# Kernel optimization log

Measured on AMD Instinct MI355X. Metric: run time of the kernel, lower is better.

The kernel has to match this reference:

```python
import jax, jax.numpy as jnp
import numpy as np

TEMP_LP = 0.05  # args.temp_lp_loss


def setup_inputs() -> dict:
    key = jax.random.key(0)
    k1, k2, k3, k4 = jax.random.split(key, 4)
    B, B_s, topk, C, n_ids = 4096, 4096, 4, 128, 751
    feats = jax.random.normal(k1, (B, C), dtype=jnp.float32)
    feats_s = jax.random.normal(k2, (B_s, topk, C), dtype=jnp.float32)
    labels = jax.random.randint(k3, (B,), 0, n_ids)
    labels_s = jax.random.randint(k4, (B_s * topk,), 0, n_ids)
    return {"feats": feats, "feats_s": feats_s, "labels": labels, "labels_s": labels_s}


def reference(feats, feats_s, labels, labels_s):
    # feats: [B, C]; feats_s: [B_s, topk, C] -> [N, C] with N = B_s*topk
    B, C = feats.shape
    fs = feats_s.reshape(-1, C)
    sim = (feats @ fs.T) / TEMP_LP                      # [B, N]
    # Per-sample: target puts weight 1/P on the P positives (labels_s == label),
    # 0 on negatives. Concatenation order does not affect log_softmax values, so
    # loss_i = -(1/P) * sum_{j in pos} (sim[i,j] - logsumexp(sim[i,:]))
    lse = jax.nn.logsumexpsim = None
    lse = jax.nn.logsumexp(sim, axis=1)                 # [B]
    pos = labels[:, None] == labels_s[None, :]          # [B, N] bool
    P = pos.sum(axis=1).astype(sim.dtype)               # [B]
    pos_sum = jnp.sum(jnp.where(pos, sim, jnp.zeros((), sim.dtype)), axis=1)
    loss_i = lse - pos_sum / P                          # [B]
    return jnp.sum(loss_i) / B
```

## Files before the change

### kernel.cpp

```cpp
#include <hip/hip_runtime.h>
#include <hip/hip_bf16.h>

#define B_ROWS 4096
#define N_COLS 16384
#define CDIM   128
#define NIDS   751
#define TEMP_INV 20.0f
#define ASCALE 28.853900817779268f
#define LN2 0.6931471805599453f

#define BM 256
#define BN 64
#define NCHUNK 64
#define COLS_PER_CHUNK (N_COLS / NCHUNK)
#define STEPS (COLS_PER_CHUNK / BN)
#define LSE_BLOCKS ((B_ROWS / BM) * NCHUNK)
#define POS_BLOCKS (N_COLS / 256)
#define NLBL NIDS

typedef __attribute__((ext_vector_type(8))) short short8;
typedef __attribute__((ext_vector_type(4))) float f32x4;
typedef __attribute__((ext_vector_type(4))) unsigned short u16x4;

#define AS1 __attribute__((address_space(1)))
#define AS3 __attribute__((address_space(3)))

__device__ __forceinline__ unsigned short f2bf(float x) {
  union { float f; unsigned u; } c; c.f = x;
  unsigned r = c.u + 0x7FFFu + ((c.u >> 16) & 1u);
  return (unsigned short)(r >> 16);
}

__global__ void prep_kernel(const float* __restrict__ feats, const float* __restrict__ fs,
                            const int* __restrict__ labels, const int* __restrict__ labels_s,
                            unsigned short* __restrict__ feats_bf, unsigned short* __restrict__ fs_bf,
                            float* __restrict__ Ftab, float* __restrict__ Pcnt,
                            float* __restrict__ acc) {
  const int bid = blockIdx.x;
  const int tid = threadIdx.x;
  if (bid < NLBL) {
    __shared__ int list[64];
    __shared__ int cnt;
    __shared__ float red[4];
    if (tid == 0) cnt = 0;
    if (bid == 0 && tid < 4) acc[tid] = 0.f;
    __syncthreads();
    const int4* lab4 = (const int4*)labels;
#pragma unroll
    for (int it = 0; it < 4; ++it) {
      int idx = it * 256 + tid;
      int4 v = lab4[idx];
      int r0 = idx * 4;
      if (v.x == bid) { int k = atomicAdd(&cnt, 1); if (k < 64) list[k] = r0; }
      if (v.y == bid) { int k = atomicAdd(&cnt, 1); if (k < 64) list[k] = r0 + 1; }
      if (v.z == bid) { int k = atomicAdd(&cnt, 1); if (k < 64) list[k] = r0 + 2; }
      if (v.w == bid) { int k = atomicAdd(&cnt, 1); if (k < 64) list[k] = r0 + 3; }
    }
    const int4* ls4 = (const int4*)labels_s;
    int c = 0;
#pragma unroll 4
    for (int it = 0; it < 16; ++it) {
      int4 v = ls4[it * 256 + tid];
      c += (v.x == bid) + (v.y == bid) + (v.z == bid) + (v.w == bid);
    }
#pragma unroll
    for (int off = 1; off < 64; off <<= 1) c += __shfl_xor(c, off, 64);
    if ((tid & 63) == 0) red[tid >> 6] = (float)c;
    __syncthreads();
    int n = min(cnt, 64);
    if (tid < CDIM) {
      float a = 0.f;
      for (int k = 0; k < n; ++k) a += feats[(size_t)list[k] * CDIM + tid];
      Ftab[(size_t)bid * CDIM + tid] = a;
    } else if (tid == CDIM) {
      Pcnt[bid] = red[0] + red[1] + red[2] + red[3];
    }
  } else {
    const int NF4 = B_ROWS * CDIM / 4;
    int idx = (bid - NLBL) * 256 + tid;
    if (idx < NF4) {
      f32x4 v = ((const f32x4*)feats)[idx];
      u16x4 o = { f2bf(v[0] * ASCALE), f2bf(v[1] * ASCALE), f2bf(v[2] * ASCALE), f2bf(v[3] * ASCALE) };
      ((u16x4*)feats_bf)[idx] = o;
    } else {
      int j = idx - NF4;
      f32x4 v = ((const f32x4*)fs)[j];
      u16x4 o = { f2bf(v[0]), f2bf(v[1]), f2bf(v[2]), f2bf(v[3]) };
      ((u16x4*)fs_bf)[j] = o;
    }
  }
}

__launch_bounds__(256, 2)
__global__ void main_kernel(const unsigned short* __restrict__ A,
                            const unsigned short* __restrict__ Bm,
                            const float* __restrict__ fs32,
                            const int* __restrict__ labels_s,
                            const float* __restrict__ Ftab, const float* __restrict__ Pcnt,
                            float* __restrict__ pmL,
                            float* __restrict__ acc) {
  __shared__ unsigned short lds[2][BN * CDIM];
  __shared__ float wsum[4];
  const int tid = threadIdx.x;

  if (blockIdx.x < POS_BLOCKS) {
    int j = blockIdx.x * 256 + tid;
    int l = labels_s[j];
    const f32x4* fr = (const f32x4*)(fs32 + (size_t)j * CDIM);
    const f32x4* Fr = (const f32x4*)(Ftab + (size_t)l * CDIM);
    float d = 0.f;
#pragma unroll
    for (int q = 0; q < CDIM / 4; ++q) {
      f32x4 a = fr[q], b = Fr[q];
      d += a[0] * b[0] + a[1] * b[1] + a[2] * b[2] + a[3] * b[3];
    }
    d /= Pcnt[l];
#pragma unroll
    for (int off = 1; off < 64; off <<= 1) d += __shfl_xor(d, off, 64);
    if ((tid & 63) == 0) wsum[tid >> 6] = d;
    __syncthreads();
    if (tid == 0) atomicAdd(&acc[1], wsum[0] + wsum[1] + wsum[2] + wsum[3]);
    return;
  }

  const int lseb = blockIdx.x - POS_BLOCKS;
  const int wv = tid >> 6, ln = tid & 63;
  const int hi = ln >> 4, lo = ln & 15;
  const int ch = lseb & (NCHUNK - 1);
  const int rb = lseb >> 6;
  const int col_base = ch * COLS_PER_CHUNK;

  const unsigned short* aptr = A + (size_t)(rb * BM + wv * 64 + lo) * CDIM + hi * 8;
  short8 afr[4][4];
#pragma unroll
  for (int rg = 0; rg < 4; ++rg)
#pragma unroll
    for (int kk = 0; kk < 4; ++kk)
      afr[rg][kk] = *(const short8*)(aptr + rg * 16 * CDIM + kk * 32);

  float m_[4][4], s_[4][4];
#pragma unroll
  for (int rg = 0; rg < 4; ++rg)
#pragma unroll
    for (int j = 0; j < 4; ++j) { m_[rg][j] = -1e30f; s_[rg][j] = 0.f; }

  auto stage = [&](int buf, int step) {
    const int c0 = col_base + step * BN;
    char* base = (char*)&lds[buf][0];
#pragma unroll
    for (int r = 0; r < 4; ++r) {
      int q = r * 256 + wv * 64 + ln;
      int row = q >> 4, cc = q & 15;
      int cs = cc ^ (row & 15);
      const unsigned short* src = Bm + (size_t)(c0 + row) * CDIM + cs * 8;
      __builtin_amdgcn_global_load_lds((AS1 const void*)src,
                                       (AS3 void*)(base + (size_t)(r * 256 + wv * 64) * 16),
                                       16, 0, 0);
    }
  };

  stage(0, 0);
  int cur = 0;
  for (int t = 0; t < STEPS; ++t) {
    if (t + 1 < STEPS) {
      stage(cur ^ 1, t + 1);
      asm volatile("s_waitcnt vmcnt(4)" ::: "memory");
    } else {
      asm volatile("s_waitcnt vmcnt(0)" ::: "memory");
    }
    __builtin_amdgcn_s_barrier();
    __builtin_amdgcn_sched_barrier(0);

    f32x4 accv[4][4];
#pragma unroll
    for (int ct = 0; ct < 4; ++ct) {
      const int rowT = ct * 16 + lo;
      short8 bf[4];
#pragma unroll
      for (int kk = 0; kk < 4; ++kk) {
        int qs = (kk * 4 + hi) ^ (rowT & 15);
        bf[kk] = *(const short8*)&lds[cur][rowT * CDIM + qs * 8];
      }
      __builtin_amdgcn_s_setprio(1);
#pragma unroll
      for (int rg = 0; rg < 4; ++rg) {
        f32x4 c4 = {0.f, 0.f, 0.f, 0.f};
#pragma unroll
        for (int kk = 0; kk < 4; ++kk)
          c4 = __builtin_amdgcn_mfma_f32_16x16x32_bf16(afr[rg][kk], bf[kk], c4, 0, 0, 0);
        accv[rg][ct] = c4;
      }
      __builtin_amdgcn_s_setprio(0);
    }

#pragma unroll
    for (int rg = 0; rg < 4; ++rg)
#pragma unroll
      for (int j = 0; j < 4; ++j) {
        float v0 = accv[rg][0][j], v1 = accv[rg][1][j];
        float v2 = accv[rg][2][j], v3 = accv[rg][3][j];
        float mx = fmaxf(fmaxf(v0, v1), fmaxf(v2, v3));
        float mn = fmaxf(m_[rg][j], mx);
        s_[rg][j] = s_[rg][j] * __builtin_amdgcn_exp2f(m_[rg][j] - mn)
                  + (__builtin_amdgcn_exp2f(v0 - mn) + __builtin_amdgcn_exp2f(v1 - mn))
                  + (__builtin_amdgcn_exp2f(v2 - mn) + __builtin_amdgcn_exp2f(v3 - mn));
        m_[rg][j] = mn;
      }

    __builtin_amdgcn_sched_barrier(0);
    __builtin_amdgcn_s_barrier();
    cur ^= 1;
  }

#pragma unroll
  for (int rg = 0; rg < 4; ++rg)
#pragma unroll
    for (int j = 0; j < 4; ++j) {
#pragma unroll
      for (int off = 1; off < 16; off <<= 1) {
        float mo = __shfl_xor(m_[rg][j], off, 64);
        float so = __shfl_xor(s_[rg][j], off, 64);
        float mn = fmaxf(m_[rg][j], mo);
        s_[rg][j] = s_[rg][j] * __builtin_amdgcn_exp2f(m_[rg][j] - mn)
                  + so * __builtin_amdgcn_exp2f(mo - mn);
        m_[rg][j] = mn;
      }
    }

  if (lo == 0) {
    int rbase = rb * BM + wv * 64 + hi * 4;
#pragma unroll
    for (int rg = 0; rg < 4; ++rg)
#pragma unroll
      for (int j = 0; j < 4; ++j) {
        int row = rbase + rg * 16 + j;
        pmL[(size_t)ch * B_ROWS + row] = m_[rg][j] + __log2f(s_[rg][j]);
      }
  }
}

__global__ void combine_kernel(const float* __restrict__ pmL,
                               float* __restrict__ acc,
                               float* __restrict__ out) {
  int row = blockIdx.x * blockDim.x + threadIdx.x;
  float L[NCHUNK];
  float mg = -1e30f;
#pragma unroll
  for (int c = 0; c < NCHUNK; ++c) {
    L[c] = pmL[c * B_ROWS + row];
    mg = fmaxf(mg, L[c]);
  }
  float sg = 0.f;
#pragma unroll
  for (int c = 0; c < NCHUNK; ++c) sg += __builtin_amdgcn_exp2f(L[c] - mg);
  float lse = LN2 * mg + logf(sg);
#pragma unroll
  for (int off = 1; off < 64; off <<= 1) lse += __shfl_xor(lse, off, 64);
  __shared__ float wsum[4];
  if ((threadIdx.x & 63) == 0) wsum[threadIdx.x >> 6] = lse;
  __syncthreads();
  if (threadIdx.x == 0) {
    atomicAdd(&acc[0], wsum[0] + wsum[1] + wsum[2] + wsum[3]);
    __threadfence();
    unsigned old = atomicAdd((unsigned*)&acc[2], 1u);
    if (old == (B_ROWS / 256) - 1) {
      float a0 = atomicAdd(&acc[0], 0.f);
      float a1 = atomicAdd(&acc[1], 0.f);
      out[0] = (a0 - TEMP_INV * a1) * (1.0f / (float)B_ROWS);
    }
  }
}

extern "C" void kernel_launch(void* const* d_in, const int* in_sizes, int n_in,
                              void* d_out, int out_size, void* d_ws, size_t ws_size,
                              hipStream_t stream) {
  const float* feats   = (const float*)d_in[0];
  const float* feats_s = (const float*)d_in[1];
  const int* labels    = (const int*)d_in[2];
  const int* labels_s  = (const int*)d_in[3];
  float* out = (float*)d_out;

  char* ws = (char*)d_ws;
  size_t off = 0;
  auto carve = [&](size_t bytes) -> char* {
    char* p = ws + off;
    off += (bytes + 255) & ~(size_t)255;
    return p;
  };
  unsigned short* feats_bf = (unsigned short*)carve((size_t)B_ROWS * CDIM * 2);
  unsigned short* fs_bf    = (unsigned short*)carve((size_t)N_COLS * CDIM * 2);
  float* Ftab = (float*)carve((size_t)NIDS * CDIM * 4);
  float* Pcnt = (float*)carve((size_t)NIDS * 4);
  float* pmL  = (float*)carve((size_t)NCHUNK * B_ROWS * 4);
  float* acc  = (float*)carve(4 * 4);

  const int NCVT = (B_ROWS * CDIM / 4 + N_COLS * CDIM / 4) / 256;
  prep_kernel<<<NLBL + NCVT, 256, 0, stream>>>(feats, feats_s, labels, labels_s,
                                               feats_bf, fs_bf, Ftab, Pcnt, acc);
  main_kernel<<<POS_BLOCKS + LSE_BLOCKS, 256, 0, stream>>>(feats_bf, fs_bf, feats_s, labels_s,
                                                           Ftab, Pcnt, pmL, acc);
  combine_kernel<<<B_ROWS / 256, 256, 0, stream>>>(pmL, acc, out);
}
```

Before: 123.9 us.

## Replace LDS-staged B tiles with per-wave register prefetch and lazy-rescale online softmax

Removes the LDS double-buffer and block barriers. Each wave now streams its own 16-column B fragments straight from global memory into registers with a one-step prefetch. The chunk count drops from 64 to 32 and waves cover independent row groups. The online logsumexp now updates the running max only when some lane's new value exceeds it by a threshold (a wave-wide vote). Otherwise it just accumulates exp2 of the difference, which saves the per-element rescale exponentials. The cost is that every wave reloads B redundantly from global or L2 instead of sharing one tile through LDS, and it adds a divergent branch.

```diff
diff --git a/kernel.cpp b/kernel.cpp
--- a/kernel.cpp
+++ b/kernel.cpp
@@ -8,22 +8,18 @@
 #define TEMP_INV 20.0f
 #define ASCALE 28.853900817779268f
 #define LN2 0.6931471805599453f
-
-#define BM 256
-#define BN 64
-#define NCHUNK 64
-#define COLS_PER_CHUNK (N_COLS / NCHUNK)
-#define STEPS (COLS_PER_CHUNK / BN)
-#define LSE_BLOCKS ((B_ROWS / BM) * NCHUNK)
+#define THR 32.0f
+
+#define NCHUNK 32
+#define CPC (N_COLS / NCHUNK)
+#define TSTEPS (CPC / 16)
+#define LSE_BLOCKS 512
 #define POS_BLOCKS (N_COLS / 256)
 #define NLBL NIDS
 
 typedef __attribute__((ext_vector_type(8))) short short8;
 typedef __attribute__((ext_vector_type(4))) float f32x4;
 typedef __attribute__((ext_vector_type(4))) unsigned short u16x4;
-
-#define AS1 __attribute__((address_space(1)))
-#define AS3 __attribute__((address_space(3)))
 
 __device__ __forceinline__ unsigned short f2bf(float x) {
   union { float f; unsigned u; } c; c.f = x;
@@ -99,11 +95,10 @@
                             const float* __restrict__ Ftab, const float* __restrict__ Pcnt,
                             float* __restrict__ pmL,
                             float* __restrict__ acc) {
-  __shared__ unsigned short lds[2][BN * CDIM];
-  __shared__ float wsum[4];
   const int tid = threadIdx.x;
 
   if (blockIdx.x < POS_BLOCKS) {
+    __shared__ float wsum[4];
     int j = blockIdx.x * 256 + tid;
     int l = labels_s[j];
     const f32x4* fr = (const f32x4*)(fs32 + (size_t)j * CDIM);
@@ -127,10 +122,10 @@
   const int wv = tid >> 6, ln = tid & 63;
   const int hi = ln >> 4, lo = ln & 15;
   const int ch = lseb & (NCHUNK - 1);
-  const int rb = lseb >> 6;
-  const int col_base = ch * COLS_PER_CHUNK;
-
-  const unsigned short* aptr = A + (size_t)(rb * BM + wv * 64 + lo) * CDIM + hi * 8;
+  const int rowg = ((lseb >> 5) << 2) | wv;
+  const int row0 = rowg * 64;
+
+  const unsigned short* aptr = A + (size_t)(row0 + lo) * CDIM + hi * 8;
   short8 afr[4][4];
 #pragma unroll
   for (int rg = 0; rg < 4; ++rg)
@@ -138,104 +133,81 @@
     for (int kk = 0; kk < 4; ++kk)
       afr[rg][kk] = *(const short8*)(aptr + rg * 16 * CDIM + kk * 32);
 
-  float m_[4][4], s_[4][4];
-#pragma unroll
-  for (int rg = 0; rg < 4; ++rg)
-#pragma unroll
-    for (int j = 0; j < 4; ++j) { m_[rg][j] = -1e30f; s_[rg][j] = 0.f; }
-
-  auto stage = [&](int buf, int step) {
-    const int c0 = col_base + step * BN;
-    char* base = (char*)&lds[buf][0];
-#pragma unroll
-    for (int r = 0; r < 4; ++r) {
-      int q = r * 256 + wv * 64 + ln;
-      int row = q >> 4, cc = q & 15;
-      int cs = cc ^ (row & 15);
-      const unsigned short* src = Bm + (size_t)(c0 + row) * CDIM + cs * 8;
-      __builtin_amdgcn_global_load_lds((AS1 const void*)src,
-                                       (AS3 void*)(base + (size_t)(r * 256 + wv * 64) * 16),
-                                       16, 0, 0);
-    }
-  };
-
-  stage(0, 0);
-  int cur = 0;
-  for (int t = 0; t < STEPS; ++t) {
-    if (t + 1 < STEPS) {
-      stage(cur ^ 1, t + 1);
-      asm volatile("s_waitcnt vmcnt(4)" ::: "memory");
+  float m_[16], s_[16];
+#pragma unroll
+  for (int g = 0; g < 16; ++g) { m_[g] = -1e30f; s_[g] = 0.f; }
+
+  const unsigned short* bptr = Bm + (size_t)(ch * CPC + lo) * CDIM + hi * 8;
+  short8 bcur[4], bnxt[4];
+#pragma unroll
+  for (int kk = 0; kk < 4; ++kk) bcur[kk] = *(const short8*)(bptr + kk * 32);
+  bptr += 16 * CDIM;
+
+  for (int t = 0; t < TSTEPS; ++t) {
+    if (t + 1 < TSTEPS) {
+#pragma unroll
+      for (int kk = 0; kk < 4; ++kk) bnxt[kk] = *(const short8*)(bptr + kk * 32);
+      bptr += 16 * CDIM;
+    }
+
+    f32x4 av[4];
+#pragma unroll
+    for (int rg = 0; rg < 4; ++rg) {
+      f32x4 c4 = {0.f, 0.f, 0.f, 0.f};
+#pragma unroll
+      for (int kk = 0; kk < 4; ++kk)
+        c4 = __builtin_amdgcn_mfma_f32_16x16x32_bf16(afr[rg][kk], bcur[kk], c4, 0, 0, 0);
+      av[rg] = c4;
+    }
+
+    float d_[16], dm = -1e30f;
+#pragma unroll
+    for (int rg = 0; rg < 4; ++rg)
+#pragma unroll
+      for (int j = 0; j < 4; ++j) {
+        d_[rg * 4 + j] = av[rg][j] - m_[rg * 4 + j];
+        dm = fmaxf(dm, d_[rg * 4 + j]);
+      }
+    if (__any(dm > THR)) {
+#pragma unroll
+      for (int rg = 0; rg < 4; ++rg)
+#pragma unroll
+        for (int j = 0; j < 4; ++j) {
+          int g = rg * 4 + j;
+          float v = av[rg][j];
+          float mn = fmaxf(m_[g], v);
+          s_[g] = s_[g] * __builtin_amdgcn_exp2f(m_[g] - mn)
+                + __builtin_amdgcn_exp2f(v - mn);
+          m_[g] = mn;
+        }
     } else {
-      asm volatile("s_waitcnt vmcnt(0)" ::: "memory");
-    }
-    __builtin_amdgcn_s_barrier();
-    __builtin_amdgcn_sched_barrier(0);
-
-    f32x4 accv[4][4];
-#pragma unroll
-    for (int ct = 0; ct < 4; ++ct) {
-      const int rowT = ct * 16 + lo;
-      short8 bf[4];
-#pragma unroll
-      for (int kk = 0; kk < 4; ++kk) {
-        int qs = (kk * 4 + hi) ^ (rowT & 15);
-        bf[kk] = *(const short8*)&lds[cur][rowT * CDIM + qs * 8];
-      }
-      __builtin_amdgcn_s_setprio(1);
-#pragma unroll
-      for (int rg = 0; rg < 4; ++rg) {
-        f32x4 c4 = {0.f, 0.f, 0.f, 0.f};
-#pragma unroll
-        for (int kk = 0; kk < 4; ++kk)
-          c4 = __builtin_amdgcn_mfma_f32_16x16x32_bf16(afr[rg][kk], bf[kk], c4, 0, 0, 0);
-        accv[rg][ct] = c4;
-      }
-      __builtin_amdgcn_s_setprio(0);
-    }
-
-#pragma unroll
-    for (int rg = 0; rg < 4; ++rg)
-#pragma unroll
-      for (int j = 0; j < 4; ++j) {
-        float v0 = accv[rg][0][j], v1 = accv[rg][1][j];
-        float v2 = accv[rg][2][j], v3 = accv[rg][3][j];
-        float mx = fmaxf(fmaxf(v0, v1), fmaxf(v2, v3));
-        float mn = fmaxf(m_[rg][j], mx);
-        s_[rg][j] = s_[rg][j] * __builtin_amdgcn_exp2f(m_[rg][j] - mn)
-                  + (__builtin_amdgcn_exp2f(v0 - mn) + __builtin_amdgcn_exp2f(v1 - mn))
-                  + (__builtin_amdgcn_exp2f(v2 - mn) + __builtin_amdgcn_exp2f(v3 - mn));
-        m_[rg][j] = mn;
-      }
-
-    __builtin_amdgcn_sched_barrier(0);
-    __builtin_amdgcn_s_barrier();
-    cur ^= 1;
-  }
-
-#pragma unroll
-  for (int rg = 0; rg < 4; ++rg)
-#pragma unroll
-    for (int j = 0; j < 4; ++j) {
-#pragma unroll
-      for (int off = 1; off < 16; off <<= 1) {
-        float mo = __shfl_xor(m_[rg][j], off, 64);
-        float so = __shfl_xor(s_[rg][j], off, 64);
-        float mn = fmaxf(m_[rg][j], mo);
-        s_[rg][j] = s_[rg][j] * __builtin_amdgcn_exp2f(m_[rg][j] - mn)
-                  + so * __builtin_amdgcn_exp2f(mo - mn);
-        m_[rg][j] = mn;
-      }
-    }
+#pragma unroll
+      for (int g = 0; g < 16; ++g) s_[g] += __builtin_amdgcn_exp2f(d_[g]);
+    }
+
+#pragma unroll
+    for (int kk = 0; kk < 4; ++kk) bcur[kk] = bnxt[kk];
+  }
+
+#pragma unroll
+  for (int off = 1; off < 16; off <<= 1) {
+#pragma unroll
+    for (int g = 0; g < 16; ++g) {
+      float mo = __shfl_xor(m_[g], off, 64);
+      float so = __shfl_xor(s_[g], off, 64);
+      float mn = fmaxf(m_[g], mo);
+      s_[g] = s_[g] * __builtin_amdgcn_exp2f(m_[g] - mn)
+            + so * __builtin_amdgcn_exp2f(mo - mn);
+      m_[g] = mn;
+    }
+  }
 
   if (lo == 0) {
-    int rbase = rb * BM + wv * 64 + hi * 4;
-#pragma unroll
-    for (int rg = 0; rg < 4; ++rg)
-#pragma unroll
-      for (int j = 0; j < 4; ++j) {
-        int row = rbase + rg * 16 + j;
-        pmL[(size_t)ch * B_ROWS + row] = m_[rg][j] + __log2f(s_[rg][j]);
-      }
+#pragma unroll
+    for (int g = 0; g < 16; ++g) {
+      int row = row0 + (g >> 2) * 16 + hi * 4 + (g & 3);
+      pmL[(size_t)ch * B_ROWS + row] = m_[g] + __log2f(s_[g]);
+    }
   }
 }
 
```

New measurement: 122.2 us. About the same (-1.4%).
